# Kernel optimization log

Hardware: AMD Instinct MI355X
Metric: run time of the kernel (lower is better)

Reference implementation:

```python
import jax, jax.numpy as jnp
import numpy as np

L = 5           # num_layer
D = 128         # emb_dim
N = 100_000     # num nodes
E = 1_600_000   # num edges
EDGE_F = 7      # raw edge feature dim
BN_EPS = 1e-5


def batchnorm(z, gamma, beta):
    # BatchNorm1d in training-style normalization: biased batch mean/var over axis 0
    mu = z.mean(axis=0)
    var = z.var(axis=0)
    return gamma * (z - mu) * jax.lax.rsqrt(var + BN_EPS) + beta


def setup_inputs() -> dict:
    key = jax.random.key(0)
    ks = jax.random.split(key, 16)
    s = 0.05
    return {
        "x": jnp.zeros((N,), jnp.int32),                               # Embedding(1, D) indices
        "edge_index": jax.random.randint(ks[0], (2, E), 0, N, jnp.int32),
        "edge_attr": jax.random.normal(ks[1], (E, EDGE_F), jnp.float32),
        "node_emb": jax.random.normal(ks[2], (1, D), jnp.float32) * s,
        "We": jax.random.normal(ks[3], (L, EDGE_F, D), jnp.float32) * s,   # edge_encoder weight
        "be": jax.random.normal(ks[4], (L, D), jnp.float32) * s,
        "eps": jnp.zeros((L,), jnp.float32),                               # GIN eps, init 0
        "W1": jax.random.normal(ks[5], (L, D, 2 * D), jnp.float32) * s,
        "b1": jax.random.normal(ks[6], (L, 2 * D), jnp.float32) * s,
        "g1": jnp.ones((L, 2 * D), jnp.float32),                           # mlp inner BN gamma
        "bt1": jnp.zeros((L, 2 * D), jnp.float32),                         # mlp inner BN beta
        "W2": jax.random.normal(ks[7], (L, 2 * D, D), jnp.float32) * s,
        "b2": jax.random.normal(ks[8], (L, D), jnp.float32) * s,
        "gbn": jnp.ones((L, D), jnp.float32),                              # outer BN gamma
        "bbn": jnp.zeros((L, D), jnp.float32),                             # outer BN beta
    }


def reference(x, edge_index, edge_attr, node_emb, We, be, eps, W1, b1, g1, bt1, W2, b2, gbn, bbn):
    # node encoder (Embedding with vocab=1)
    h = node_emb[x]                       # [N, D]
    src, dst = edge_index[0], edge_index[1]
    for l in range(L):
        # edge embedding + GIN message: relu(x_j + edge_emb), scatter-add at dst
        ee = edge_attr @ We[l] + be[l]                       # [E, D]
        msg = jax.nn.relu(h[src] + ee)                       # gather + add + relu
        agg = jax.ops.segment_sum(msg, dst, num_segments=N)  # scatter-add
        out = (1.0 + eps[l]) * h + agg                       # [N, D]
        # mlp: Linear(D,2D) -> BN -> ReLU -> Linear(2D,D)
        z = batchnorm(out @ W1[l] + b1[l], g1[l], bt1[l])
        z = jax.nn.relu(z) @ W2[l] + b2[l]
        # outer BatchNorm; dropout is identity in eval mode
        h = batchnorm(z, gbn[l], bbn[l])
        if l < L - 1:
            h = jax.nn.relu(h)
    return h
```

## Files before the change

kernel.cpp:

```cpp
#include <hip/hip_runtime.h>
#include <cstddef>

#define NN 100000
#define NE 1600000
#define D 128
#define D2 256
#define EF 7
#define NL 5
#define BN_EPS 1e-5f
#define GW 12500
#define SCAN_NB ((NN + 1023) / 1024)

typedef unsigned short ushort_t;
typedef __attribute__((ext_vector_type(8))) _Float16 f16x8;
typedef __attribute__((ext_vector_type(2))) _Float16 h2v;
typedef __attribute__((ext_vector_type(4))) float f32x4;

__device__ __forceinline__ void atomAddF(float* p, float v) { unsafeAtomicAdd(p, v); }

__device__ __forceinline__ ushort_t f2h(float f) {
    return __builtin_bit_cast(ushort_t, (_Float16)f);
}
__device__ __forceinline__ unsigned pk2h(float lo, float hi) {
    return (unsigned)f2h(lo) | ((unsigned)f2h(hi) << 16);
}
__device__ __forceinline__ float h2f(unsigned u16) {
    return (float)__builtin_bit_cast(_Float16, (ushort_t)(u16 & 0xFFFFu));
}
__device__ __forceinline__ h2v u2h2(unsigned u) { return __builtin_bit_cast(h2v, u); }

__global__ __launch_bounds__(256)
void hist_kernel(const int* __restrict__ ei, int* __restrict__ counts)
{
    const int e = blockIdx.x * 256 + threadIdx.x;
    if (e < NE) atomicAdd(&counts[ei[NE + e]], 1);
}

__global__ __launch_bounds__(256)
void scanA_kernel(const int* __restrict__ counts, int* __restrict__ bsum)
{
    __shared__ int sred[256];
    const int t = threadIdx.x;
    const int base = blockIdx.x * 1024 + t * 4;
    int s = 0;
    #pragma unroll
    for (int j = 0; j < 4; ++j) { const int i = base + j; if (i < NN) s += counts[i]; }
    sred[t] = s;
    __syncthreads();
    for (int off = 128; off > 0; off >>= 1) {
        if (t < off) sred[t] += sred[t + off];
        __syncthreads();
    }
    if (t == 0) bsum[blockIdx.x] = sred[0];
}

__global__ __launch_bounds__(128)
void scanB_kernel(const int* __restrict__ bsum, int* __restrict__ bbase,
                  int* __restrict__ offs)
{
    __shared__ int ss[128];
    const int t = threadIdx.x;
    const int v = (t < SCAN_NB) ? bsum[t] : 0;
    ss[t] = v;
    __syncthreads();
    for (int off = 1; off < 128; off <<= 1) {
        int u = 0;
        if (t >= off) u = ss[t - off];
        __syncthreads();
        ss[t] += u;
        __syncthreads();
    }
    if (t < SCAN_NB) bbase[t] = ss[t] - v;
    if (t == 0) offs[NN] = NE;
}

__global__ __launch_bounds__(256)
void scanC_kernel(const int* __restrict__ counts, const int* __restrict__ bbase,
                  int* __restrict__ offs)
{
    __shared__ int sts[256];
    const int t = threadIdx.x;
    const int base = blockIdx.x * 1024 + t * 4;
    int c[4];
    int s = 0;
    #pragma unroll
    for (int j = 0; j < 4; ++j) {
        const int i = base + j;
        c[j] = (i < NN) ? counts[i] : 0;
        s += c[j];
    }
    sts[t] = s;
    __syncthreads();
    for (int off = 1; off < 256; off <<= 1) {
        int u = 0;
        if (t >= off) u = sts[t - off];
        __syncthreads();
        sts[t] += u;
        __syncthreads();
    }
    int run = bbase[blockIdx.x] + sts[t] - s;
    #pragma unroll
    for (int j = 0; j < 4; ++j) {
        const int i = base + j;
        if (i < NN) { offs[i] = run; run += c[j]; }
    }
}

__global__ __launch_bounds__(256)
void scatter_kernel(const int* __restrict__ ei, const float* __restrict__ ea,
                    int* __restrict__ offmut, int* __restrict__ sSrc,
                    ushort_t* __restrict__ eaH)
{
    const int e = blockIdx.x * 256 + threadIdx.x;
    if (e < NE) {
        const int dst = ei[NE + e];
        const int pos = atomicAdd(&offmut[dst], 1);
        sSrc[pos] = ei[e];
        const float* eap = &ea[(size_t)e * EF];
        const unsigned o0 = pk2h(eap[0], eap[1]);
        const unsigned o1 = pk2h(eap[2], eap[3]);
        const unsigned o2 = pk2h(eap[4], eap[5]);
        const unsigned o3 = pk2h(eap[6], 0.f);
        *(uint4*)&eaH[(size_t)pos * 8] = make_uint4(o0, o1, o2, o3);
    }
}

__global__ __launch_bounds__(256)
void wconv_kernel(const float* __restrict__ W1, const float* __restrict__ W2,
                  ushort_t* __restrict__ W1t, ushort_t* __restrict__ W2t)
{
    const int idx = blockIdx.x * 256 + threadIdx.x;
    const int per = D * D2;
    if (idx < NL * per) {
        const int l = idx / per, r = idx % per;
        const int k1 = r / D2, n1 = r % D2;
        W1t[(size_t)l * per + n1 * D + k1] = f2h(W1[idx]);
        const int k2 = r / D, n2 = r % D;
        W2t[(size_t)l * per + n2 * D2 + k2] = f2h(W2[idx]);
    }
}

template<int L0>
__global__ __launch_bounds__(256)
void gather_kernel(const int* __restrict__ offs, const int* __restrict__ sSrc,
                   const ushort_t* __restrict__ eaH,
                   const float* __restrict__ We, const float* __restrict__ be,
                   const ushort_t* __restrict__ hAct, const float* __restrict__ h0,
                   const float* __restrict__ epsp,
                   ushort_t* __restrict__ xinH, float* __restrict__ xsum)
{
    __shared__ __align__(16) float sCS[4][D];
    const int lane = threadIdx.x & 63;
    const int w = threadIdx.x >> 6;
    const int wid = blockIdx.x * 4 + w;

    const float2* We2 = (const float2*)We;
    const unsigned* hU = (const unsigned*)hAct;
    unsigned* xU = (unsigned*)xinH;
    h2v wP[EF];
    #pragma unroll
    for (int k = 0; k < EF; ++k) {
        const float2 wf = We2[k * 64 + lane];
        wP[k] = (h2v){(_Float16)wf.x, (_Float16)wf.y};
    }
    h2v beP;
    {
        const float2 bf = ((const float2*)be)[lane];
        beP = (h2v){(_Float16)bf.x, (_Float16)bf.y};
    }
    float2 h0v = {0.f, 0.f};
    h2v h0P = (h2v){(_Float16)0.f, (_Float16)0.f};
    if (L0) {
        h0v = ((const float2*)h0)[lane];
        h0P = (h2v){(_Float16)h0v.x, (_Float16)h0v.y};
    }
    const float epsv = 1.0f + *epsp;
    const h2v zz = (h2v){(_Float16)0.f, (_Float16)0.f};

    int p4[8], e4[8];
    #pragma unroll
    for (int i = 0; i < 8; ++i) {
        const int n = wid + i * GW;
        p4[i] = __builtin_amdgcn_readfirstlane(offs[n]);
        e4[i] = __builtin_amdgcn_readfirstlane(offs[n + 1]);
    }
    int mx = 0;
    #pragma unroll
    for (int i = 0; i < 8; ++i) mx = max(mx, e4[i] - p4[i]);

    float2 acc[8];
    #pragma unroll
    for (int i = 0; i < 8; ++i) acc[i] = (float2){0.f, 0.f};

    for (int j = 0; j < mx; ++j) {
        unsigned hwd[8];
        uint4 ev4[8];
        bool on[8];
        #pragma unroll
        for (int i = 0; i < 8; ++i) {
            on[i] = p4[i] < e4[i];
            if (on[i]) {
                ev4[i] = *(const uint4*)&eaH[(size_t)p4[i] * 8];
                if (!L0) {
                    const int src = sSrc[p4[i]];
                    hwd[i] = hU[(src << 6) + lane];
                }
            }
        }
        #pragma unroll
        for (int i = 0; i < 8; ++i) {
            if (on[i]) {
                const h2v e01 = u2h2(ev4[i].x);
                const h2v e23 = u2h2(ev4[i].y);
                const h2v e45 = u2h2(ev4[i].z);
                const h2v e6x = u2h2(ev4[i].w);
                h2v m = beP;
                m = __builtin_elementwise_fma(__builtin_shufflevector(e01, e01, 0, 0), wP[0], m);
                m = __builtin_elementwise_fma(__builtin_shufflevector(e01, e01, 1, 1), wP[1], m);
                m = __builtin_elementwise_fma(__builtin_shufflevector(e23, e23, 0, 0), wP[2], m);
                m = __builtin_elementwise_fma(__builtin_shufflevector(e23, e23, 1, 1), wP[3], m);
                m = __builtin_elementwise_fma(__builtin_shufflevector(e45, e45, 0, 0), wP[4], m);
                m = __builtin_elementwise_fma(__builtin_shufflevector(e45, e45, 1, 1), wP[5], m);
                m = __builtin_elementwise_fma(__builtin_shufflevector(e6x, e6x, 0, 0), wP[6], m);
                const h2v hh = L0 ? h0P : u2h2(hwd[i]);
                const h2v r = __builtin_elementwise_max(m + hh, zz);
                acc[i].x += (float)r.x;
                acc[i].y += (float)r.y;
                ++p4[i];
            }
        }
    }

    float2 cs = {0.f, 0.f};
    #pragma unroll
    for (int i = 0; i < 8; ++i) {
        const int n = wid + i * GW;
        float2 hs;
        if (L0) hs = h0v;
        else {
            const unsigned hv = hU[(n << 6) + lane];
            hs.x = h2f(hv); hs.y = h2f(hv >> 16);
        }
        float2 a = acc[i];
        a.x = fmaf(epsv, hs.x, a.x);
        a.y = fmaf(epsv, hs.y, a.y);
        cs.x += a.x; cs.y += a.y;
        xU[(n << 6) + lane] = pk2h(a.x, a.y);
    }
    sCS[w][2 * lane] = cs.x;
    sCS[w][2 * lane + 1] = cs.y;
    __syncthreads();
    if (threadIdx.x < D) {
        atomAddF(&xsum[threadIdx.x],
                 sCS[0][threadIdx.x] + sCS[1][threadIdx.x] +
                 sCS[2][threadIdx.x] + sCS[3][threadIdx.x]);
    }
}

__global__ __launch_bounds__(256, 2)
void mm1_kernel(const ushort_t* __restrict__ xinH, const float* __restrict__ xsum,
                const ushort_t* __restrict__ W1t,
                ushort_t* __restrict__ z1H, float* __restrict__ stats)
{
    __shared__ __align__(16) ushort_t sA[64 * 128];
    __shared__ __align__(16) float sM[D];
    const int t = threadIdx.x;
    if (t < D) sM[t] = xsum[t] * (1.0f / (float)NN);
    const int i0 = blockIdx.x * 64;
    const int lane = t & 63, w = t >> 6;
    const int nb = w * 64;

    f16x8 bfr[4][4];
    #pragma unroll
    for (int nt = 0; nt < 4; ++nt)
        #pragma unroll
        for (int ks = 0; ks < 4; ++ks) {
            const int n = nb + nt * 16 + (lane & 15);
            const int k = ks * 32 + (lane >> 4) * 8;
            bfr[nt][ks] = *(const f16x8*)&W1t[n * D + k];
        }
    __syncthreads();

    #pragma unroll
    for (int p = 0; p < 4; ++p) {
        const int linear = p * 256 + t;
        const int row = linear >> 4, ch = linear & 15;
        const int gi = i0 + row;
        unsigned oo[4] = {0, 0, 0, 0};
        if (gi < NN) {
            const uint4 v = *(const uint4*)&xinH[(size_t)gi * D + ch * 8];
            const unsigned uu[4] = {v.x, v.y, v.z, v.w};
            #pragma unroll
            for (int j2 = 0; j2 < 4; ++j2) {
                const int c0 = ch * 8 + j2 * 2;
                oo[j2] = pk2h(h2f(uu[j2]) - sM[c0], h2f(uu[j2] >> 16) - sM[c0 + 1]);
            }
        }
        unsigned boff = (unsigned)(row * 256 + ch * 16);
        boff ^= (unsigned)((row & 7) << 4);
        *(uint4*)((char*)sA + boff) = make_uint4(oo[0], oo[1], oo[2], oo[3]);
    }
    __syncthreads();

    f32x4 acc[4][4];
    #pragma unroll
    for (int a = 0; a < 4; ++a)
        #pragma unroll
        for (int b = 0; b < 4; ++b) acc[a][b] = (f32x4){0.f, 0.f, 0.f, 0.f};

    #pragma unroll
    for (int mt = 0; mt < 4; ++mt) {
        f16x8 af[4];
        #pragma unroll
        for (int ks = 0; ks < 4; ++ks) {
            const int row = mt * 16 + (lane & 15);
            unsigned boff = (unsigned)(row * 256 + ks * 64 + (lane >> 4) * 16);
            boff ^= (unsigned)((row & 7) << 4);
            af[ks] = *(const f16x8*)((const char*)sA + boff);
        }
        #pragma unroll
        for (int nt = 0; nt < 4; ++nt)
            #pragma unroll
            for (int ks = 0; ks < 4; ++ks)
                acc[mt][nt] = __builtin_amdgcn_mfma_f32_16x16x32_f16(af[ks], bfr[nt][ks], acc[mt][nt], 0, 0, 0);
    }

    float s[4], q[4];
    #pragma unroll
    for (int nt = 0; nt < 4; ++nt) { s[nt] = 0.f; q[nt] = 0.f; }
    #pragma unroll
    for (int nt = 0; nt < 4; ++nt) {
        const int n = nb + nt * 16 + (lane & 15);
        #pragma unroll
        for (int mt = 0; mt < 4; ++mt)
            #pragma unroll
            for (int r = 0; r < 4; ++r) {
                const int i = i0 + mt * 16 + (lane >> 4) * 4 + r;
                if (i < NN) {
                    const float v = acc[mt][nt][r];
                    s[nt] += v; q[nt] = fmaf(v, v, q[nt]);
                    z1H[(size_t)i * D2 + n] = f2h(v);
                }
            }
    }
    #pragma unroll
    for (int nt = 0; nt < 4; ++nt) {
        s[nt] += __shfl_xor(s[nt], 16, 64); s[nt] += __shfl_xor(s[nt], 32, 64);
        q[nt] += __shfl_xor(q[nt], 16, 64); q[nt] += __shfl_xor(q[nt], 32, 64);
    }
    if (lane < 16) {
        #pragma unroll
        for (int nt = 0; nt < 4; ++nt) {
            const int n = nb + nt * 16 + lane;
            atomAddF(&stats[n], s[nt]);
            atomAddF(&stats[D2 + n], q[nt]);
        }
    }
}

__global__ __launch_bounds__(256, 2)
void mm2_kernel(const ushort_t* __restrict__ z1H, const float* __restrict__ stats1,
                const float* __restrict__ g1, const float* __restrict__ bt1,
                const ushort_t* __restrict__ W2t,
                ushort_t* __restrict__ z2H, float* __restrict__ stats2)
{
    __shared__ __align__(16) ushort_t sA[64 * 256];
    __shared__ __align__(16) float sAff[2 * D2];
    __shared__ __align__(16) float sYm[D2];
    const int t = threadIdx.x;
    {
        const float inv = 1.0f / (float)NN;
        const float mu = stats1[t] * inv;
        const float var = fmaf(-mu, mu, stats1[D2 + t] * inv);
        const float a = g1[t] * rsqrtf(var + BN_EPS);
        sAff[t] = a;
        sAff[D2 + t] = fmaf(-a, mu, bt1[t]);
        const float m0 = bt1[t];
        const float sg = fabsf(g1[t]);
        float ym;
        if (sg > 1e-20f) {
            const float r = m0 / sg;
            const float Ph = 0.5f * (1.0f + erff(r * 0.70710678f));
            const float ph = 0.39894228f * expf(-0.5f * r * r);
            ym = m0 * Ph + sg * ph;
        } else {
            ym = fmaxf(m0, 0.f);
        }
        sYm[t] = ym;
    }
    const int i0 = blockIdx.x * 64;
    const int lane = t & 63, w = t >> 6;
    const int nb = w * 32;

    f16x8 bfr[2][8];
    #pragma unroll
    for (int nt = 0; nt < 2; ++nt)
        #pragma unroll
        for (int ks = 0; ks < 8; ++ks) {
            const int n = nb + nt * 16 + (lane & 15);
            const int k = ks * 32 + (lane >> 4) * 8;
            bfr[nt][ks] = *(const f16x8*)&W2t[n * D2 + k];
        }
    __syncthreads();

    #pragma unroll
    for (int p = 0; p < 8; ++p) {
        const int linear = p * 256 + t;
        const int row = linear >> 5, ch = linear & 31;
        const int gi = i0 + row;
        unsigned oo[4] = {0, 0, 0, 0};
        if (gi < NN) {
            const uint4 v = *(const uint4*)&z1H[(size_t)gi * D2 + ch * 8];
            const unsigned uu[4] = {v.x, v.y, v.z, v.w};
            #pragma unroll
            for (int j2 = 0; j2 < 4; ++j2) {
                const int c0 = ch * 8 + j2 * 2;
                float lo = h2f(uu[j2]);
                float hi = h2f(uu[j2] >> 16);
                lo = fmaxf(fmaf(sAff[c0], lo, sAff[D2 + c0]), 0.f) - sYm[c0];
                hi = fmaxf(fmaf(sAff[c0 + 1], hi, sAff[D2 + c0 + 1]), 0.f) - sYm[c0 + 1];
                oo[j2] = pk2h(lo, hi);
            }
        }
        unsigned boff = (unsigned)(row * 512 + ch * 16);
        boff ^= (unsigned)((row & 7) << 4);
        *(uint4*)((char*)sA + boff) = make_uint4(oo[0], oo[1], oo[2], oo[3]);
    }
    __syncthreads();

    f32x4 acc[4][2];
    #pragma unroll
    for (int a = 0; a < 4; ++a)
        #pragma unroll
        for (int b = 0; b < 2; ++b) acc[a][b] = (f32x4){0.f, 0.f, 0.f, 0.f};

    #pragma unroll
    for (int mt = 0; mt < 4; ++mt) {
        f16x8 af[8];
        #pragma unroll
        for (int ks = 0; ks < 8; ++ks) {
            const int row = mt * 16 + (lane & 15);
            unsigned boff = (unsigned)(row * 512 + ks * 64 + (lane >> 4) * 16);
            boff ^= (unsigned)((row & 7) << 4);
            af[ks] = *(const f16x8*)((const char*)sA + boff);
        }
        #pragma unroll
        for (int nt = 0; nt < 2; ++nt)
            #pragma unroll
            for (int ks = 0; ks < 8; ++ks)
                acc[mt][nt] = __builtin_amdgcn_mfma_f32_16x16x32_f16(af[ks], bfr[nt][ks], acc[mt][nt], 0, 0, 0);
    }

    float s[2], q[2];
    #pragma unroll
    for (int nt = 0; nt < 2; ++nt) { s[nt] = 0.f; q[nt] = 0.f; }
    #pragma unroll
    for (int nt = 0; nt < 2; ++nt) {
        const int n = nb + nt * 16 + (lane & 15);
        #pragma unroll
        for (int mt = 0; mt < 4; ++mt)
            #pragma unroll
            for (int r = 0; r < 4; ++r) {
                const int i = i0 + mt * 16 + (lane >> 4) * 4 + r;
                if (i < NN) {
                    const float v = acc[mt][nt][r];
                    s[nt] += v; q[nt] = fmaf(v, v, q[nt]);
                    z2H[(size_t)i * D + n] = f2h(v);
                }
            }
    }
    #pragma unroll
    for (int nt = 0; nt < 2; ++nt) {
        s[nt] += __shfl_xor(s[nt], 16, 64); s[nt] += __shfl_xor(s[nt], 32, 64);
        q[nt] += __shfl_xor(q[nt], 16, 64); q[nt] += __shfl_xor(q[nt], 32, 64);
    }
    if (lane < 16) {
        #pragma unroll
        for (int nt = 0; nt < 2; ++nt) {
            const int n = nb + nt * 16 + lane;
            atomAddF(&stats2[n], s[nt]);
            atomAddF(&stats2[D + n], q[nt]);
        }
    }
}

template<int HALF>
__global__ __launch_bounds__(256)
void act_kernel(const ushort_t* __restrict__ z2H, const float* __restrict__ stats2,
                const float* __restrict__ g, const float* __restrict__ bt,
                void* __restrict__ dstv)
{
    __shared__ float sA[D], sC[D];
    const int t = threadIdx.x;
    if (t < D) {
        const float inv = 1.0f / (float)NN;
        const float mu = stats2[t] * inv;
        const float var = fmaf(-mu, mu, stats2[D + t] * inv);
        const float a = g[t] * rsqrtf(var + BN_EPS);
        sA[t] = a;
        sC[t] = fmaf(-a, mu, bt[t]);
    }
    __syncthreads();
    const int idx = blockIdx.x * 256 + t;
    if (idx < NN * D / 4) {
        const int d0 = (idx * 4) & (D - 1);
        const uint2 v = *(const uint2*)&z2H[(size_t)idx * 4];
        float4 o;
        o.x = fmaf(sA[d0 + 0], h2f(v.x),       sC[d0 + 0]);
        o.y = fmaf(sA[d0 + 1], h2f(v.x >> 16), sC[d0 + 1]);
        o.z = fmaf(sA[d0 + 2], h2f(v.y),       sC[d0 + 2]);
        o.w = fmaf(sA[d0 + 3], h2f(v.y >> 16), sC[d0 + 3]);
        if (HALF) {
            o.x = fmaxf(o.x, 0.f); o.y = fmaxf(o.y, 0.f);
            o.z = fmaxf(o.z, 0.f); o.w = fmaxf(o.w, 0.f);
            uint2 pkd;
            pkd.x = pk2h(o.x, o.y);
            pkd.y = pk2h(o.z, o.w);
            *((uint2*)dstv + idx) = pkd;
        } else {
            *((float4*)dstv + idx) = o;
        }
    }
}

extern "C" void kernel_launch(void* const* d_in, const int* in_sizes, int n_in,
                              void* d_out, int out_size, void* d_ws, size_t ws_size,
                              hipStream_t stream)
{
    (void)in_sizes; (void)n_in; (void)out_size; (void)ws_size;
    const int*   ei       = (const int*)d_in[1];
    const float* ea       = (const float*)d_in[2];
    const float* node_emb = (const float*)d_in[3];
    const float* We       = (const float*)d_in[4];
    const float* be       = (const float*)d_in[5];
    const float* eps      = (const float*)d_in[6];
    const float* W1       = (const float*)d_in[7];
    const float* g1       = (const float*)d_in[9];
    const float* bt1      = (const float*)d_in[10];
    const float* W2       = (const float*)d_in[11];
    const float* gbn      = (const float*)d_in[13];
    const float* bbn      = (const float*)d_in[14];
    float* out = (float*)d_out;

    char* base = (char*)d_ws;
    size_t off = 0;
    auto alloc = [&](size_t bytes) -> void* {
        void* p = base + off;
        off = (off + bytes + 255) & ~(size_t)255;
        return p;
    };
    ushort_t* tmpH   = (ushort_t*)alloc((size_t)NN * D * 2);
    ushort_t* z1H    = (ushort_t*)alloc((size_t)NN * D2 * 2);
    ushort_t* hAct   = (ushort_t*)alloc((size_t)NN * D * 2);
    ushort_t* W1t    = (ushort_t*)alloc((size_t)NL * D * D2 * 2);
    ushort_t* W2t    = (ushort_t*)alloc((size_t)NL * D * D2 * 2);
    float*    red    = (float*)alloc(896 * sizeof(float));
    float*    stats1 = red;
    float*    stats2 = red + 512;
    float*    xsum   = red + 768;
    int*      counts = (int*)alloc((NN + 1) * sizeof(int));
    int*      offs   = (int*)alloc((NN + 1) * sizeof(int));
    int*      offmut = (int*)alloc(NN * sizeof(int));
    int*      bsum   = (int*)alloc(SCAN_NB * sizeof(int));
    int*      bbase  = (int*)alloc(SCAN_NB * sizeof(int));
    int*      sSrc   = (int*)alloc((size_t)NE * sizeof(int));
    ushort_t* eaH    = (ushort_t*)alloc((size_t)NE * 8 * 2);

    hipMemsetAsync(counts, 0, (NN + 1) * sizeof(int), stream);
    hist_kernel<<<(NE + 255) / 256, 256, 0, stream>>>(ei, counts);
    scanA_kernel<<<SCAN_NB, 256, 0, stream>>>(counts, bsum);
    scanB_kernel<<<1, 128, 0, stream>>>(bsum, bbase, offs);
    scanC_kernel<<<SCAN_NB, 256, 0, stream>>>(counts, bbase, offs);
    hipMemcpyAsync(offmut, offs, NN * sizeof(int), hipMemcpyDeviceToDevice, stream);
    scatter_kernel<<<(NE + 255) / 256, 256, 0, stream>>>(ei, ea, offmut, sSrc, eaH);
    wconv_kernel<<<(NL * D * D2 + 255) / 256, 256, 0, stream>>>(W1, W2, W1t, W2t);

    for (int l = 0; l < NL; ++l) {
        hipMemsetAsync(red, 0, 896 * sizeof(float), stream);
        if (l == 0) {
            gather_kernel<1><<<GW / 4, 256, 0, stream>>>(offs, sSrc, eaH,
                                                         We + l * EF * D, be + l * D,
                                                         hAct, node_emb, eps + l, tmpH, xsum);
        } else {
            gather_kernel<0><<<GW / 4, 256, 0, stream>>>(offs, sSrc, eaH,
                                                         We + l * EF * D, be + l * D,
                                                         hAct, node_emb, eps + l, tmpH, xsum);
        }
        mm1_kernel<<<(NN + 63) / 64, 256, 0, stream>>>(tmpH, xsum, W1t + (size_t)l * D * D2,
                                                       z1H, stats1);
        mm2_kernel<<<(NN + 63) / 64, 256, 0, stream>>>(z1H, stats1, g1 + l * D2, bt1 + l * D2,
                                                       W2t + (size_t)l * D * D2,
                                                       tmpH, stats2);
        if (l < NL - 1) {
            act_kernel<1><<<(NN * D / 4 + 255) / 256, 256, 0, stream>>>(
                tmpH, stats2, gbn + l * D, bbn + l * D, hAct);
        } else {
            act_kernel<0><<<(NN * D / 4 + 255) / 256, 256, 0, stream>>>(
                tmpH, stats2, gbn + l * D, bbn + l * D, out);
        }
    }
}
```

Measured before the change: 1.606 ms.

## Fuse outer BatchNorm+ReLU into next layer's gather and batch per-layer stat buffers

Removes the intermediate act_kernel for layers 0-3 by folding the outer BatchNorm affine and ReLU into the gather kernel, which now reads raw z2 and applies a*z+c then max(0) per neighbour and per self term. Stats buffers become per-layer so a single upfront memset replaces five per-layer memsets, and the offmut copy is folded into scanC. This saves a full read/write pass over the N×D activation per layer plus several launches, at the cost of redoing the BN affine for every edge read in the gather (extra fp16 FMA per message) and computing the BN coefficients in fp16.

```diff
diff --git a/kernel.cpp b/kernel.cpp
--- a/kernel.cpp
+++ b/kernel.cpp
@@ -76,7 +76,7 @@
 
 __global__ __launch_bounds__(256)
 void scanC_kernel(const int* __restrict__ counts, const int* __restrict__ bbase,
-                  int* __restrict__ offs)
+                  int* __restrict__ offs, int* __restrict__ offmut)
 {
     __shared__ int sts[256];
     const int t = threadIdx.x;
@@ -102,7 +102,7 @@
     #pragma unroll
     for (int j = 0; j < 4; ++j) {
         const int i = base + j;
-        if (i < NN) { offs[i] = run; run += c[j]; }
+        if (i < NN) { offs[i] = run; offmut[i] = run; run += c[j]; }
     }
 }
 
@@ -145,8 +145,9 @@
 void gather_kernel(const int* __restrict__ offs, const int* __restrict__ sSrc,
                    const ushort_t* __restrict__ eaH,
                    const float* __restrict__ We, const float* __restrict__ be,
-                   const ushort_t* __restrict__ hAct, const float* __restrict__ h0,
-                   const float* __restrict__ epsp,
+                   const ushort_t* __restrict__ z2H, const float* __restrict__ stats2p,
+                   const float* __restrict__ gbn, const float* __restrict__ bbn,
+                   const float* __restrict__ h0, const float* __restrict__ epsp,
                    ushort_t* __restrict__ xinH, float* __restrict__ xsum)
 {
     __shared__ __align__(16) float sCS[4][D];
@@ -155,7 +156,7 @@
     const int wid = blockIdx.x * 4 + w;
 
     const float2* We2 = (const float2*)We;
-    const unsigned* hU = (const unsigned*)hAct;
+    const unsigned* hU = (const unsigned*)z2H;
     unsigned* xU = (unsigned*)xinH;
     h2v wP[EF];
     #pragma unroll
@@ -170,9 +171,24 @@
     }
     float2 h0v = {0.f, 0.f};
     h2v h0P = (h2v){(_Float16)0.f, (_Float16)0.f};
+    h2v aP = (h2v){(_Float16)0.f, (_Float16)0.f};
+    h2v cP = (h2v){(_Float16)0.f, (_Float16)0.f};
     if (L0) {
         h0v = ((const float2*)h0)[lane];
         h0P = (h2v){(_Float16)h0v.x, (_Float16)h0v.y};
+    } else {
+        const float inv = 1.0f / (float)NN;
+        const int c0i = 2 * lane, c1i = 2 * lane + 1;
+        const float mu0 = stats2p[c0i] * inv;
+        const float mu1 = stats2p[c1i] * inv;
+        const float v0 = fmaf(-mu0, mu0, stats2p[D + c0i] * inv);
+        const float v1 = fmaf(-mu1, mu1, stats2p[D + c1i] * inv);
+        const float a0 = gbn[c0i] * rsqrtf(v0 + BN_EPS);
+        const float a1 = gbn[c1i] * rsqrtf(v1 + BN_EPS);
+        const float c0 = fmaf(-a0, mu0, bbn[c0i]);
+        const float c1 = fmaf(-a1, mu1, bbn[c1i]);
+        aP = (h2v){(_Float16)a0, (_Float16)a1};
+        cP = (h2v){(_Float16)c0, (_Float16)c1};
     }
     const float epsv = 1.0f + *epsp;
     const h2v zz = (h2v){(_Float16)0.f, (_Float16)0.f};
@@ -222,7 +238,10 @@
                 m = __builtin_elementwise_fma(__builtin_shufflevector(e45, e45, 0, 0), wP[4], m);
                 m = __builtin_elementwise_fma(__builtin_shufflevector(e45, e45, 1, 1), wP[5], m);
                 m = __builtin_elementwise_fma(__builtin_shufflevector(e6x, e6x, 0, 0), wP[6], m);
-                const h2v hh = L0 ? h0P : u2h2(hwd[i]);
+                h2v hh;
+                if (L0) hh = h0P;
+                else hh = __builtin_elementwise_max(
+                         __builtin_elementwise_fma(aP, u2h2(hwd[i]), cP), zz);
                 const h2v r = __builtin_elementwise_max(m + hh, zz);
                 acc[i].x += (float)r.x;
                 acc[i].y += (float)r.y;
@@ -238,8 +257,9 @@
         float2 hs;
         if (L0) hs = h0v;
         else {
-            const unsigned hv = hU[(n << 6) + lane];
-            hs.x = h2f(hv); hs.y = h2f(hv >> 16);
+            const h2v hz = __builtin_elementwise_max(
+                __builtin_elementwise_fma(aP, u2h2(hU[(n << 6) + lane]), cP), zz);
+            hs.x = (float)hz.x; hs.y = (float)hz.y;
         }
         float2 a = acc[i];
         a.x = fmaf(epsv, hs.x, a.x);
@@ -484,11 +504,10 @@
     }
 }
 
-template<int HALF>
 __global__ __launch_bounds__(256)
 void act_kernel(const ushort_t* __restrict__ z2H, const float* __restrict__ stats2,
                 const float* __restrict__ g, const float* __restrict__ bt,
-                void* __restrict__ dstv)
+                float* __restrict__ out)
 {
     __shared__ float sA[D], sC[D];
     const int t = threadIdx.x;
@@ -510,16 +529,7 @@
         o.y = fmaf(sA[d0 + 1], h2f(v.x >> 16), sC[d0 + 1]);
         o.z = fmaf(sA[d0 + 2], h2f(v.y),       sC[d0 + 2]);
         o.w = fmaf(sA[d0 + 3], h2f(v.y >> 16), sC[d0 + 3]);
-        if (HALF) {
-            o.x = fmaxf(o.x, 0.f); o.y = fmaxf(o.y, 0.f);
-            o.z = fmaxf(o.z, 0.f); o.w = fmaxf(o.w, 0.f);
-            uint2 pkd;
-            pkd.x = pk2h(o.x, o.y);
-            pkd.y = pk2h(o.z, o.w);
-            *((uint2*)dstv + idx) = pkd;
-        } else {
-            *((float4*)dstv + idx) = o;
-        }
+        *(float4*)&out[(size_t)idx * 4] = o;
     }
 }
 
@@ -549,15 +559,12 @@
         off = (off + bytes + 255) & ~(size_t)255;
         return p;
     };
-    ushort_t* tmpH   = (ushort_t*)alloc((size_t)NN * D * 2);
+    ushort_t* xinH   = (ushort_t*)alloc((size_t)NN * D * 2);
     ushort_t* z1H    = (ushort_t*)alloc((size_t)NN * D2 * 2);
-    ushort_t* hAct   = (ushort_t*)alloc((size_t)NN * D * 2);
+    ushort_t* z2H    = (ushort_t*)alloc((size_t)NN * D * 2);
     ushort_t* W1t    = (ushort_t*)alloc((size_t)NL * D * D2 * 2);
     ushort_t* W2t    = (ushort_t*)alloc((size_t)NL * D * D2 * 2);
-    float*    red    = (float*)alloc(896 * sizeof(float));
-    float*    stats1 = red;
-    float*    stats2 = red + 512;
-    float*    xsum   = red + 768;
+    float*    red    = (float*)alloc((size_t)NL * 896 * sizeof(float));
     int*      counts = (int*)alloc((NN + 1) * sizeof(int));
     int*      offs   = (int*)alloc((NN + 1) * sizeof(int));
     int*      offmut = (int*)alloc(NN * sizeof(int));
@@ -567,36 +574,37 @@
     ushort_t* eaH    = (ushort_t*)alloc((size_t)NE * 8 * 2);
 
     hipMemsetAsync(counts, 0, (NN + 1) * sizeof(int), stream);
+    hipMemsetAsync(red, 0, (size_t)NL * 896 * sizeof(float), stream);
     hist_kernel<<<(NE + 255) / 256, 256, 0, stream>>>(ei, counts);
     scanA_kernel<<<SCAN_NB, 256, 0, stream>>>(counts, bsum);
     scanB_kernel<<<1, 128, 0, stream>>>(bsum, bbase, offs);
-    scanC_kernel<<<SCAN_NB, 256, 0, stream>>>(counts, bbase, offs);
-    hipMemcpyAsync(offmut, offs, NN * sizeof(int), hipMemcpyDeviceToDevice, stream);
+    scanC_kernel<<<SCAN_NB, 256, 0, stream>>>(counts, bbase, offs, offmut);
     scatter_kernel<<<(NE + 255) / 256, 256, 0, stream>>>(ei, ea, offmut, sSrc, eaH);
     wconv_kernel<<<(NL * D * D2 + 255) / 256, 256, 0, stream>>>(W1, W2, W1t, W2t);
 
     for (int l = 0; l < NL; ++l) {
-        hipMemsetAsync(red, 0, 896 * sizeof(float), stream);
+        float* redl   = red + (size_t)l * 896;
+        float* stats1 = redl;
+        float* stats2 = redl + 512;
+        float* xsum   = redl + 768;
         if (l == 0) {
             gather_kernel<1><<<GW / 4, 256, 0, stream>>>(offs, sSrc, eaH,
-                                                         We + l * EF * D, be + l * D,
-                                                         hAct, node_emb, eps + l, tmpH, xsum);
+                We + l * EF * D, be + l * D,
+                z2H, nullptr, nullptr, nullptr,
+                node_emb, eps + l, xinH, xsum);
         } else {
+            const float* stats2p = red + (size_t)(l - 1) * 896 + 512;
             gather_kernel<0><<<GW / 4, 256, 0, stream>>>(offs, sSrc, eaH,
-                                                         We + l * EF * D, be + l * D,
-                                                         hAct, node_emb, eps + l, tmpH, xsum);
-        }
-        mm1_kernel<<<(NN + 63) / 64, 256, 0, stream>>>(tmpH, xsum, W1t + (size_t)l * D * D2,
+                We + l * EF * D, be + l * D,
+                z2H, stats2p, gbn + (l - 1) * D, bbn + (l - 1) * D,
+                node_emb, eps + l, xinH, xsum);
+        }
+        mm1_kernel<<<(NN + 63) / 64, 256, 0, stream>>>(xinH, xsum, W1t + (size_t)l * D * D2,
                                                        z1H, stats1);
         mm2_kernel<<<(NN + 63) / 64, 256, 0, stream>>>(z1H, stats1, g1 + l * D2, bt1 + l * D2,
                                                        W2t + (size_t)l * D * D2,
-                                                       tmpH, stats2);
-        if (l < NL - 1) {
-            act_kernel<1><<<(NN * D / 4 + 255) / 256, 256, 0, stream>>>(
-                tmpH, stats2, gbn + l * D, bbn + l * D, hAct);
-        } else {
-            act_kernel<0><<<(NN * D / 4 + 255) / 256, 256, 0, stream>>>(
-                tmpH, stats2, gbn + l * D, bbn + l * D, out);
-        }
-    }
-}
+                                                       z2H, stats2);
+    }
+    act_kernel<<<(NN * D / 4 + 255) / 256, 256, 0, stream>>>(
+        z2H, red + (size_t)(NL - 1) * 896 + 512, gbn + (NL - 1) * D, bbn + (NL - 1) * D, out);
+}
```

Result: faster. 1.557 ms, median of 2 (-3.1%).
